# Performance work log

Measured on AMD Instinct MI355X. Metric: run time of the kernel, lower is better.

## Reference

```python
import jax, jax.numpy as jnp
import numpy as np

B, L, C = 131072, 50, 3
WIN = 10  # running std window


def setup_inputs() -> dict:
    key = jax.random.key(0)
    ks = jax.random.split(key, 12)
    def xavier(k, shape, fan_in, fan_out, gain):
        bound = gain * np.sqrt(6.0 / (fan_in + fan_out))
        return jax.random.uniform(k, shape, jnp.float32, -bound, bound)
    relu_g = np.sqrt(2.0)
    return {
        "signal": jax.random.normal(ks[0], (B, L, C), jnp.float32),
        # conv weights: (out_ch, in_ch, kernel)
        "conv1_w": xavier(ks[1], (5, 3, 3), 3 * 3, 5 * 3, relu_g),
        "conv1_b": jnp.zeros((5,), jnp.float32),
        "conv2_w": xavier(ks[2], (10, 5, 3), 5 * 3, 10 * 3, relu_g),
        "conv2_b": jnp.zeros((10,), jnp.float32),
        "fc1_w": xavier(ks[3], (256, 360), 360, 256, relu_g),
        "fc1_b": jnp.zeros((256,), jnp.float32),
        "fc2_w": xavier(ks[4], (64, 256), 256, 64, relu_g),
        "fc2_b": jnp.zeros((64,), jnp.float32),
        "pamap_w": xavier(ks[5], (12, 64), 64, 12, 1.0),
        "pamap_b": jnp.zeros((12,), jnp.float32),
    }


def running_std(x, w):
    # x: (B, L, C) -> (B, L - w, C); unbiased std (ddof=1) over sliding window,
    # computed with prefix sums instead of per-window kernels.
    b, l, c = x.shape
    z = jnp.zeros((b, 1, c), x.dtype)
    cs = jnp.concatenate([z, jnp.cumsum(x, axis=1)], axis=1)
    cs2 = jnp.concatenate([z, jnp.cumsum(x * x, axis=1)], axis=1)
    lo = l - w  # note: torch loop produces L - w windows (last window dropped)
    s = cs[:, w:w + lo] - cs[:, :lo]
    s2 = cs2[:, w:w + lo] - cs2[:, :lo]
    var = (s2 - s * s / w) / (w - 1)
    return jnp.sqrt(jnp.maximum(var, 0.0))


def conv1d(x, w, b):
    # x: (B, C, T), w: (O, I, K)
    y = jax.lax.conv_general_dilated(x, w, (1,), 'VALID',
                                     dimension_numbers=('NCH', 'OIH', 'NCH'))
    return y + b[None, :, None]


def reference(signal, conv1_w, conv1_b, conv2_w, conv2_b,
              fc1_w, fc1_b, fc2_w, fc2_b, pamap_w, pamap_b):
    sd = running_std(signal, WIN)            # (B, 40, 3)
    x = jnp.transpose(sd, (0, 2, 1))          # (B, 3, 40)
    h = jax.nn.relu(conv1d(x, conv1_w, conv1_b))   # (B, 5, 38)
    h = jax.nn.relu(conv1d(h, conv2_w, conv2_b))   # (B, 10, 36)
    flat = jnp.transpose(h, (0, 2, 1)).reshape(-1, 36 * 10)  # (B, 360)
    f = jax.nn.relu(flat @ fc1_w.T + fc1_b)
    f = jax.nn.relu(f @ fc2_w.T + fc2_b)
    logits = f @ pamap_w.T + pamap_b           # flag=False -> pamap head
    return jax.nn.log_softmax(logits, axis=1)
```

## Files before the change

### kernel.cpp

```cpp
#include <hip/hip_runtime.h>
#include <hip/hip_bf16.h>

typedef __attribute__((ext_vector_type(8))) short bf16x8;
typedef __attribute__((ext_vector_type(4))) float f32x4;
typedef __attribute__((ext_vector_type(8))) unsigned short u16x8;

static __device__ __forceinline__ unsigned short bf16bits(float v) {
    __hip_bfloat16 h = __float2bfloat16(v);
    return *(unsigned short*)&h;
}

__global__ __launch_bounds__(256) void prep_weights(
    const float* __restrict__ fc1w, const float* __restrict__ fc2w,
    __hip_bfloat16* __restrict__ w1o, __hip_bfloat16* __restrict__ w2o)
{
    int id = blockIdx.x * 256 + threadIdx.x;
    if (id < 256 * 384) {
        int n = id / 384, k2 = id - n * 384;
        float v = 0.0f;
        if (k2 < 360) {
            int o = k2 / 36, t = k2 - o * 36;
            v = fc1w[n * 360 + t * 10 + o];
        }
        w1o[id] = __float2bfloat16(v);
    } else {
        int id2 = id - 256 * 384;
        if (id2 < 64 * 256) w2o[id2] = __float2bfloat16(fc2w[id2]);
    }
}

#define P_BASE  0
#define P_TILE  10496
#define P_SSTR  656
#define SD_BASE 20992
#define SD_TILE 11008
#define SD_SSTR 688
#define F_BASE  20992
#define F_RSTR  784
#define CW_OFF  46080
__global__ __launch_bounds__(256, 3) void features_kernel(
    const float* __restrict__ sig,
    const float* __restrict__ c1w_g, const float* __restrict__ c1b_g,
    const float* __restrict__ c2w_g, const float* __restrict__ c2b_g,
    __hip_bfloat16* __restrict__ Fg)
{
    __shared__ __align__(16) unsigned char smem[46920];
    float* cw = (float*)(smem + CW_OFF);

    const int tid  = threadIdx.x;
    const int blk  = blockIdx.x;
    const int wv   = tid >> 6;
    const int lane = tid & 63;
    const int ml   = lane & 15;
    const int kg   = lane >> 4;

    {
        f32x4 z = {0.f, 0.f, 0.f, 0.f};
        for (int i = tid; i < 2688; i += 256)
            *(f32x4*)(smem + i * 16) = z;
        if (tid < 210) {
            float v;
            if (tid < 45)       v = c1w_g[tid];
            else if (tid < 50)  v = c1b_g[tid - 45];
            else if (tid < 200) v = c2w_g[tid - 50];
            else                v = c2b_g[tid - 200];
            cw[tid] = v;
        }
    }
    __syncthreads();

    if (tid < 192) {
        int s = tid / 6, r = tid - s * 6;
        int c = r >> 1, h = r & 1;
        int j0 = h * 20;
        const float* g = sig + (size_t)blk * 4800 + s * 150 + c;
        float x[30];
        #pragma unroll
        for (int j = 0; j < 30; ++j) x[j] = g[(j0 + j) * 3];
        float sum = 0.f, sq = 0.f;
        #pragma unroll
        for (int j = 0; j < 10; ++j) { sum += x[j]; sq += x[j] * x[j]; }
        unsigned char* sd = smem + SD_BASE + (s >> 4) * SD_TILE + (s & 15) * SD_SSTR + c * 2;
        #pragma unroll
        for (int i = 0; i < 20; ++i) {
            float var = (sq - sum * sum * 0.1f) * (1.0f / 9.0f);
            *(unsigned short*)(sd + (j0 + i) * 16) = bf16bits(sqrtf(fmaxf(var, 0.f)));
            if (i < 19) {
                float d = x[i + 10] - x[i];
                sq  += d * (x[i + 10] + x[i]);
                sum += d;
            }
        }
    }

    bf16x8 B1f, B2f;
    #pragma unroll
    for (int j = 0; j < 8; ++j) {
        float v1 = (ml < 5  && kg < 3 && j < 3) ? cw[ml * 9 + j * 3 + kg] : 0.f;
        float v2 = (ml < 10 && kg < 3 && j < 5) ? cw[50 + ml * 15 + j * 3 + kg] : 0.f;
        B1f[j] = (short)bf16bits(v1);
        B2f[j] = (short)bf16bits(v2);
    }
    const float c1bias = (ml < 5)  ? cw[45 + ml]  : 0.f;
    const float c2bias = (ml < 10) ? cw[200 + ml] : 0.f;
    __syncthreads();

    {
        const int tile = wv >> 1, half = wv & 1;
        const unsigned char* sdb = smem + SD_BASE + tile * SD_TILE + ml * SD_SSTR;
        unsigned char* pb = smem + P_BASE + tile * P_TILE + ml * 2;
        #pragma unroll
        for (int it = 0; it < 19; ++it) {
            int t = half * 19 + it;
            bf16x8 a = *(const bf16x8*)(sdb + (t + kg) * 16);
            f32x4 acc = {0.f, 0.f, 0.f, 0.f};
            acc = __builtin_amdgcn_mfma_f32_16x16x32_bf16(a, B1f, acc, 0, 0, 0);
            if (ml < 5) {
                #pragma unroll
                for (int i = 0; i < 4; ++i) {
                    float v = fmaxf(acc[i] + c1bias, 0.f);
                    *(unsigned short*)(pb + (kg * 4 + i) * P_SSTR + t * 16) = bf16bits(v);
                }
            }
        }
    }
    __syncthreads();

    if (tid < 128) {
        f32x4 z = {0.f, 0.f, 0.f, 0.f};
        int r = tid >> 2, q = tid & 3;
        *(f32x4*)(smem + F_BASE + r * F_RSTR + 720 + q * 16) = z;
    }

    {
        const int tile = wv >> 1, half = wv & 1;
        const unsigned char* pbr = smem + P_BASE + tile * P_TILE + ml * P_SSTR;
        unsigned char* fb = smem + F_BASE + tile * 16 * F_RSTR + ml * 72;
        #pragma unroll
        for (int it = 0; it < 18; ++it) {
            int t = half * 18 + it;
            bf16x8 a = *(const bf16x8*)(pbr + (t + kg) * 16);
            f32x4 acc = {0.f, 0.f, 0.f, 0.f};
            acc = __builtin_amdgcn_mfma_f32_16x16x32_bf16(a, B2f, acc, 0, 0, 0);
            if (ml < 10) {
                #pragma unroll
                for (int i = 0; i < 4; ++i) {
                    float v = fmaxf(acc[i] + c2bias, 0.f);
                    *(unsigned short*)(fb + (kg * 4 + i) * F_RSTR + t * 2) = bf16bits(v);
                }
            }
        }
    }
    __syncthreads();

    {
        u16x8* dstv = (u16x8*)Fg + (size_t)blk * 1536;
        for (int i = tid; i < 1536; i += 256) {
            int r = i / 48, cc = i - r * 48;
            dstv[i] = *(const u16x8*)(smem + F_BASE + r * F_RSTR + cc * 16);
        }
    }
}

__global__ __launch_bounds__(256, 2) void fc_head_kernel(
    const __hip_bfloat16* __restrict__ Fg,
    const __hip_bfloat16* __restrict__ W1, const __hip_bfloat16* __restrict__ W2,
    const float* __restrict__ fc1b, const float* __restrict__ fc2b,
    const float* __restrict__ pw, const float* __restrict__ pb,
    float* __restrict__ out)
{
    __shared__ __align__(16) unsigned char smem[63536];
    float* pwl = (float*)(smem + 60416);
    float* pbl = (float*)(smem + 63488);

    const int tid  = threadIdx.x;
    const int blk  = blockIdx.x;
    const int w    = tid >> 6;
    const int lane = tid & 63;
    const int ml   = lane & 15;
    const int kg   = lane >> 4;
    unsigned char* Tw = smem + 50176 + w * 2560;

    for (int i = tid; i < 780; i += 256) {
        if (i < 768) pwl[i] = pw[i]; else pbl[i - 768] = pb[i - 768];
    }

    const __hip_bfloat16* myF = Fg + (size_t)(blk * 128 + w * 32 + ml) * 384;
    bf16x8 bfr[12][2];
    #pragma unroll
    for (int kk = 0; kk < 12; ++kk) {
        bfr[kk][0] = *(const bf16x8*)(myF + kk * 32 + kg * 8);
        bfr[kk][1] = *(const bf16x8*)(myF + 16 * 384 + kk * 32 + kg * 8);
    }

    {
        const u16x8* src = (const u16x8*)W1;
        __hip_bfloat16* b0 = (__hip_bfloat16*)smem;
        #pragma unroll
        for (int it = 0; it < 6; ++it) {
            int v = tid + it * 256;
            int n = v / 48, k8 = v - n * 48;
            *(u16x8*)(b0 + n * 392 + k8 * 8) = src[v];
        }
    }
    bf16x8 a2f[4];
    #pragma unroll
    for (int t2 = 0; t2 < 4; ++t2)
        a2f[t2] = *(const bf16x8*)(W2 + (t2 * 16 + ml) * 256 + kg * 8);

    f32x4 acc2[4][2];
    #pragma unroll
    for (int t2 = 0; t2 < 4; ++t2) {
        acc2[t2][0] = f32x4{0, 0, 0, 0};
        acc2[t2][1] = f32x4{0, 0, 0, 0};
    }

    for (int c = 0; c < 8; ++c) {
        __syncthreads();
        const __hip_bfloat16* cur = (const __hip_bfloat16*)(smem + (c & 1) * 25088);

        u16x8 nf[6];
        bf16x8 a2n[4];
        if (c < 7) {
            const u16x8* src = (const u16x8*)(W1 + (c + 1) * 32 * 384);
            #pragma unroll
            for (int it = 0; it < 6; ++it) nf[it] = src[tid + it * 256];
            #pragma unroll
            for (int t2 = 0; t2 < 4; ++t2)
                a2n[t2] = *(const bf16x8*)(W2 + (t2 * 16 + ml) * 256 + (c + 1) * 32 + kg * 8);
        }

        f32x4 a1acc[2][2];
        #pragma unroll
        for (int rt = 0; rt < 2; ++rt) {
            a1acc[rt][0] = f32x4{0, 0, 0, 0};
            a1acc[rt][1] = f32x4{0, 0, 0, 0};
        }
        #pragma unroll
        for (int kk = 0; kk < 12; ++kk) {
            bf16x8 w0 = *(const bf16x8*)(cur + ml * 392 + kk * 32 + kg * 8);
            bf16x8 w1 = *(const bf16x8*)(cur + (16 + ml) * 392 + kk * 32 + kg * 8);
            a1acc[0][0] = __builtin_amdgcn_mfma_f32_16x16x32_bf16(w0, bfr[kk][0], a1acc[0][0], 0, 0, 0);
            a1acc[0][1] = __builtin_amdgcn_mfma_f32_16x16x32_bf16(w0, bfr[kk][1], a1acc[0][1], 0, 0, 0);
            a1acc[1][0] = __builtin_amdgcn_mfma_f32_16x16x32_bf16(w1, bfr[kk][0], a1acc[1][0], 0, 0, 0);
            a1acc[1][1] = __builtin_amdgcn_mfma_f32_16x16x32_bf16(w1, bfr[kk][1], a1acc[1][1], 0, 0, 0);
        }

        #pragma unroll
        for (int rt = 0; rt < 2; ++rt) {
            float4 b4 = *(const float4*)(fc1b + c * 32 + rt * 16 + kg * 4);
            #pragma unroll
            for (int st = 0; st < 2; ++st) {
                unsigned int p0 =
                    (unsigned int)bf16bits(fmaxf(a1acc[rt][st][0] + b4.x, 0.f))
                  | ((unsigned int)bf16bits(fmaxf(a1acc[rt][st][1] + b4.y, 0.f)) << 16);
                unsigned int p1 =
                    (unsigned int)bf16bits(fmaxf(a1acc[rt][st][2] + b4.z, 0.f))
                  | ((unsigned int)bf16bits(fmaxf(a1acc[rt][st][3] + b4.w, 0.f)) << 16);
                uint2 pk = {p0, p1};
                *(uint2*)(Tw + (st * 16 + ml) * 80 + (rt * 16 + kg * 4) * 2) = pk;
            }
        }
        asm volatile("s_waitcnt lgkmcnt(0)" ::: "memory");
        __builtin_amdgcn_sched_barrier(0);

        bf16x8 pf0 = *(const bf16x8*)(Tw + ml * 80 + kg * 16);
        bf16x8 pf1 = *(const bf16x8*)(Tw + (16 + ml) * 80 + kg * 16);
        #pragma unroll
        for (int t2 = 0; t2 < 4; ++t2) {
            acc2[t2][0] = __builtin_amdgcn_mfma_f32_16x16x32_bf16(a2f[t2], pf0, acc2[t2][0], 0, 0, 0);
            acc2[t2][1] = __builtin_amdgcn_mfma_f32_16x16x32_bf16(a2f[t2], pf1, acc2[t2][1], 0, 0, 0);
        }

        if (c < 7) {
            __hip_bfloat16* nxt = (__hip_bfloat16*)(smem + ((c + 1) & 1) * 25088);
            #pragma unroll
            for (int it = 0; it < 6; ++it) {
                int v = tid + it * 256;
                int n = v / 48, k8 = v - n * 48;
                *(u16x8*)(nxt + n * 392 + k8 * 8) = nf[it];
            }
            #pragma unroll
            for (int t2 = 0; t2 < 4; ++t2) a2f[t2] = a2n[t2];
        }
    }

    #pragma unroll
    for (int st = 0; st < 2; ++st) {
        float h[16];
        #pragma unroll
        for (int t2 = 0; t2 < 4; ++t2) {
            float4 b4 = *(const float4*)(fc2b + t2 * 16 + kg * 4);
            #pragma unroll
            for (int i = 0; i < 4; ++i)
                h[t2 * 4 + i] = fmaxf(acc2[t2][st][i] + ((const float*)&b4)[i], 0.f);
        }
        float lg[12];
        #pragma unroll
        for (int j = 0; j < 12; ++j) {
            float s = 0.f;
            #pragma unroll
            for (int t2 = 0; t2 < 4; ++t2) {
                float4 wv4 = *(const float4*)(pwl + j * 64 + t2 * 16 + kg * 4);
                s += wv4.x * h[t2 * 4 + 0] + wv4.y * h[t2 * 4 + 1]
                   + wv4.z * h[t2 * 4 + 2] + wv4.w * h[t2 * 4 + 3];
            }
            lg[j] = s;
        }
        #pragma unroll
        for (int j = 0; j < 12; ++j) {
            lg[j] += __shfl_xor(lg[j], 16);
            lg[j] += __shfl_xor(lg[j], 32);
            lg[j] += pbl[j];
        }
        float m = lg[0];
        #pragma unroll
        for (int j = 1; j < 12; ++j) m = fmaxf(m, lg[j]);
        float e = 0.f;
        #pragma unroll
        for (int j = 0; j < 12; ++j) e += __expf(lg[j] - m);
        float lse = m + __logf(e);
        if (kg == 0) {
            float* op = out + (size_t)(blk * 128 + w * 32 + st * 16 + ml) * 12;
            float4 o0 = {lg[0] - lse, lg[1] - lse, lg[2]  - lse, lg[3]  - lse};
            float4 o1 = {lg[4] - lse, lg[5] - lse, lg[6]  - lse, lg[7]  - lse};
            float4 o2 = {lg[8] - lse, lg[9] - lse, lg[10] - lse, lg[11] - lse};
            ((float4*)op)[0] = o0; ((float4*)op)[1] = o1; ((float4*)op)[2] = o2;
        }
    }
}

extern "C" void kernel_launch(void* const* d_in, const int* in_sizes, int n_in,
                              void* d_out, int out_size, void* d_ws, size_t ws_size,
                              hipStream_t stream) {
    const float* sig = (const float*)d_in[0];
    const float* c1w = (const float*)d_in[1];
    const float* c1b = (const float*)d_in[2];
    const float* c2w = (const float*)d_in[3];
    const float* c2b = (const float*)d_in[4];
    const float* f1w = (const float*)d_in[5];
    const float* f1b = (const float*)d_in[6];
    const float* f2w = (const float*)d_in[7];
    const float* f2b = (const float*)d_in[8];
    const float* pw  = (const float*)d_in[9];
    const float* pb  = (const float*)d_in[10];
    float* out = (float*)d_out;

    __hip_bfloat16* W1 = (__hip_bfloat16*)d_ws;
    __hip_bfloat16* W2 = (__hip_bfloat16*)((char*)d_ws + 196608);
    __hip_bfloat16* Fg = (__hip_bfloat16*)((char*)d_ws + 229376);

    prep_weights<<<448, 256, 0, stream>>>(f1w, f2w, W1, W2);
    features_kernel<<<4096, 256, 0, stream>>>(sig, c1w, c1b, c2w, c2b, Fg);
    fc_head_kernel<<<1024, 256, 0, stream>>>(Fg, W1, W2, f1b, f2b, pw, pb, out);
}
```

Before: 219.8 us.

## Fuse conv feature kernel with FC head to drop feature round-trip

Merges the features kernel and the FC head kernel into one launch. The bf16 feature tile now stays in LDS and feeds the fc1 MFMA directly, with fc1 output going through LDS to fc2 and the softmax head. This removes the global write and read of the 131072x384 feature matrix and one kernel launch. In exchange, each block now handles only 32 rows and reads the full fc1 weight straight from global/L2 with no LDS staging, so weight traffic per row rises. Only two of the four waves do the fc2 stage, which may leave the CU underused there.

```diff
diff --git a/kernel.cpp b/kernel.cpp
--- a/kernel.cpp
+++ b/kernel.cpp
@@ -38,14 +38,27 @@
 #define F_BASE  20992
 #define F_RSTR  784
 #define CW_OFF  46080
-__global__ __launch_bounds__(256, 3) void features_kernel(
+#define B1B_OFF 46920
+#define B2B_OFF 47944
+#define PW_OFF  48200
+#define PB_OFF  51272
+#define T_BASE  0
+#define T_SSTR  528
+__global__ __launch_bounds__(256, 3) void fused_kernel(
     const float* __restrict__ sig,
     const float* __restrict__ c1w_g, const float* __restrict__ c1b_g,
     const float* __restrict__ c2w_g, const float* __restrict__ c2b_g,
-    __hip_bfloat16* __restrict__ Fg)
+    const __hip_bfloat16* __restrict__ W1, const __hip_bfloat16* __restrict__ W2,
+    const float* __restrict__ fc1b, const float* __restrict__ fc2b,
+    const float* __restrict__ pw, const float* __restrict__ pb,
+    float* __restrict__ out)
 {
-    __shared__ __align__(16) unsigned char smem[46920];
-    float* cw = (float*)(smem + CW_OFF);
+    __shared__ __align__(16) unsigned char smem[51320];
+    float* cw  = (float*)(smem + CW_OFF);
+    float* bb1 = (float*)(smem + B1B_OFF);
+    float* bb2 = (float*)(smem + B2B_OFF);
+    float* pwl = (float*)(smem + PW_OFF);
+    float* pbl = (float*)(smem + PB_OFF);
 
     const int tid  = threadIdx.x;
     const int blk  = blockIdx.x;
@@ -66,6 +79,10 @@
             else                v = c2b_g[tid - 200];
             cw[tid] = v;
         }
+        bb1[tid] = fc1b[tid];
+        if (tid < 64) bb2[tid] = fc2b[tid];
+        for (int i = tid; i < 768; i += 256) pwl[i] = pw[i];
+        if (tid < 12) pbl[tid] = pb[tid];
     }
     __syncthreads();
 
@@ -108,7 +125,7 @@
     {
         const int tile = wv >> 1, half = wv & 1;
         const unsigned char* sdb = smem + SD_BASE + tile * SD_TILE + ml * SD_SSTR;
-        unsigned char* pb = smem + P_BASE + tile * P_TILE + ml * 2;
+        unsigned char* pbuf = smem + P_BASE + tile * P_TILE + ml * 2;
         #pragma unroll
         for (int it = 0; it < 19; ++it) {
             int t = half * 19 + it;
@@ -119,7 +136,7 @@
                 #pragma unroll
                 for (int i = 0; i < 4; ++i) {
                     float v = fmaxf(acc[i] + c1bias, 0.f);
-                    *(unsigned short*)(pb + (kg * 4 + i) * P_SSTR + t * 16) = bf16bits(v);
+                    *(unsigned short*)(pbuf + (kg * 4 + i) * P_SSTR + t * 16) = bf16bits(v);
                 }
             }
         }
@@ -153,147 +170,67 @@
     }
     __syncthreads();
 
-    {
-        u16x8* dstv = (u16x8*)Fg + (size_t)blk * 1536;
-        for (int i = tid; i < 1536; i += 256) {
-            int r = i / 48, cc = i - r * 48;
-            dstv[i] = *(const u16x8*)(smem + F_BASE + r * F_RSTR + cc * 16);
-        }
-    }
-}
-
-__global__ __launch_bounds__(256, 2) void fc_head_kernel(
-    const __hip_bfloat16* __restrict__ Fg,
-    const __hip_bfloat16* __restrict__ W1, const __hip_bfloat16* __restrict__ W2,
-    const float* __restrict__ fc1b, const float* __restrict__ fc2b,
-    const float* __restrict__ pw, const float* __restrict__ pb,
-    float* __restrict__ out)
-{
-    __shared__ __align__(16) unsigned char smem[63536];
-    float* pwl = (float*)(smem + 60416);
-    float* pbl = (float*)(smem + 63488);
-
-    const int tid  = threadIdx.x;
-    const int blk  = blockIdx.x;
-    const int w    = tid >> 6;
-    const int lane = tid & 63;
-    const int ml   = lane & 15;
-    const int kg   = lane >> 4;
-    unsigned char* Tw = smem + 50176 + w * 2560;
-
-    for (int i = tid; i < 780; i += 256) {
-        if (i < 768) pwl[i] = pw[i]; else pbl[i - 768] = pb[i - 768];
-    }
-
-    const __hip_bfloat16* myF = Fg + (size_t)(blk * 128 + w * 32 + ml) * 384;
     bf16x8 bfr[12][2];
     #pragma unroll
     for (int kk = 0; kk < 12; ++kk) {
-        bfr[kk][0] = *(const bf16x8*)(myF + kk * 32 + kg * 8);
-        bfr[kk][1] = *(const bf16x8*)(myF + 16 * 384 + kk * 32 + kg * 8);
-    }
-
-    {
-        const u16x8* src = (const u16x8*)W1;
-        __hip_bfloat16* b0 = (__hip_bfloat16*)smem;
-        #pragma unroll
-        for (int it = 0; it < 6; ++it) {
-            int v = tid + it * 256;
-            int n = v / 48, k8 = v - n * 48;
-            *(u16x8*)(b0 + n * 392 + k8 * 8) = src[v];
-        }
-    }
-    bf16x8 a2f[4];
-    #pragma unroll
-    for (int t2 = 0; t2 < 4; ++t2)
-        a2f[t2] = *(const bf16x8*)(W2 + (t2 * 16 + ml) * 256 + kg * 8);
-
-    f32x4 acc2[4][2];
-    #pragma unroll
-    for (int t2 = 0; t2 < 4; ++t2) {
-        acc2[t2][0] = f32x4{0, 0, 0, 0};
-        acc2[t2][1] = f32x4{0, 0, 0, 0};
-    }
-
-    for (int c = 0; c < 8; ++c) {
-        __syncthreads();
-        const __hip_bfloat16* cur = (const __hip_bfloat16*)(smem + (c & 1) * 25088);
-
-        u16x8 nf[6];
-        bf16x8 a2n[4];
-        if (c < 7) {
-            const u16x8* src = (const u16x8*)(W1 + (c + 1) * 32 * 384);
-            #pragma unroll
-            for (int it = 0; it < 6; ++it) nf[it] = src[tid + it * 256];
-            #pragma unroll
-            for (int t2 = 0; t2 < 4; ++t2)
-                a2n[t2] = *(const bf16x8*)(W2 + (t2 * 16 + ml) * 256 + (c + 1) * 32 + kg * 8);
-        }
-
-        f32x4 a1acc[2][2];
-        #pragma unroll
-        for (int rt = 0; rt < 2; ++rt) {
-            a1acc[rt][0] = f32x4{0, 0, 0, 0};
-            a1acc[rt][1] = f32x4{0, 0, 0, 0};
-        }
-        #pragma unroll
-        for (int kk = 0; kk < 12; ++kk) {
-            bf16x8 w0 = *(const bf16x8*)(cur + ml * 392 + kk * 32 + kg * 8);
-            bf16x8 w1 = *(const bf16x8*)(cur + (16 + ml) * 392 + kk * 32 + kg * 8);
-            a1acc[0][0] = __builtin_amdgcn_mfma_f32_16x16x32_bf16(w0, bfr[kk][0], a1acc[0][0], 0, 0, 0);
-            a1acc[0][1] = __builtin_amdgcn_mfma_f32_16x16x32_bf16(w0, bfr[kk][1], a1acc[0][1], 0, 0, 0);
-            a1acc[1][0] = __builtin_amdgcn_mfma_f32_16x16x32_bf16(w1, bfr[kk][0], a1acc[1][0], 0, 0, 0);
-            a1acc[1][1] = __builtin_amdgcn_mfma_f32_16x16x32_bf16(w1, bfr[kk][1], a1acc[1][1], 0, 0, 0);
-        }
-
-        #pragma unroll
-        for (int rt = 0; rt < 2; ++rt) {
-            float4 b4 = *(const float4*)(fc1b + c * 32 + rt * 16 + kg * 4);
-            #pragma unroll
-            for (int st = 0; st < 2; ++st) {
-                unsigned int p0 =
-                    (unsigned int)bf16bits(fmaxf(a1acc[rt][st][0] + b4.x, 0.f))
-                  | ((unsigned int)bf16bits(fmaxf(a1acc[rt][st][1] + b4.y, 0.f)) << 16);
-                unsigned int p1 =
-                    (unsigned int)bf16bits(fmaxf(a1acc[rt][st][2] + b4.z, 0.f))
-                  | ((unsigned int)bf16bits(fmaxf(a1acc[rt][st][3] + b4.w, 0.f)) << 16);
+        bfr[kk][0] = *(const bf16x8*)(smem + F_BASE + ml * F_RSTR + kk * 64 + kg * 16);
+        bfr[kk][1] = *(const bf16x8*)(smem + F_BASE + (16 + ml) * F_RSTR + kk * 64 + kg * 16);
+    }
+    {
+        const int rowbase = wv * 64;
+        #pragma unroll
+        for (int rt = 0; rt < 4; ++rt) {
+            int row0 = rowbase + rt * 16;
+            const __hip_bfloat16* wsrc = W1 + (size_t)(row0 + ml) * 384 + kg * 8;
+            f32x4 a0 = {0.f, 0.f, 0.f, 0.f}, a1 = {0.f, 0.f, 0.f, 0.f};
+            #pragma unroll
+            for (int kk = 0; kk < 12; ++kk) {
+                bf16x8 wf = *(const bf16x8*)(wsrc + kk * 32);
+                a0 = __builtin_amdgcn_mfma_f32_16x16x32_bf16(wf, bfr[kk][0], a0, 0, 0, 0);
+                a1 = __builtin_amdgcn_mfma_f32_16x16x32_bf16(wf, bfr[kk][1], a1, 0, 0, 0);
+            }
+            float4 b4 = *(const float4*)(bb1 + row0 + kg * 4);
+            {
+                unsigned int p0 = (unsigned int)bf16bits(fmaxf(a0[0] + b4.x, 0.f))
+                                | ((unsigned int)bf16bits(fmaxf(a0[1] + b4.y, 0.f)) << 16);
+                unsigned int p1 = (unsigned int)bf16bits(fmaxf(a0[2] + b4.z, 0.f))
+                                | ((unsigned int)bf16bits(fmaxf(a0[3] + b4.w, 0.f)) << 16);
                 uint2 pk = {p0, p1};
-                *(uint2*)(Tw + (st * 16 + ml) * 80 + (rt * 16 + kg * 4) * 2) = pk;
-            }
-        }
-        asm volatile("s_waitcnt lgkmcnt(0)" ::: "memory");
-        __builtin_amdgcn_sched_barrier(0);
-
-        bf16x8 pf0 = *(const bf16x8*)(Tw + ml * 80 + kg * 16);
-        bf16x8 pf1 = *(const bf16x8*)(Tw + (16 + ml) * 80 + kg * 16);
+                *(uint2*)(smem + T_BASE + ml * T_SSTR + (row0 + kg * 4) * 2) = pk;
+            }
+            {
+                unsigned int p0 = (unsigned int)bf16bits(fmaxf(a1[0] + b4.x, 0.f))
+                                | ((unsigned int)bf16bits(fmaxf(a1[1] + b4.y, 0.f)) << 16);
+                unsigned int p1 = (unsigned int)bf16bits(fmaxf(a1[2] + b4.z, 0.f))
+                                | ((unsigned int)bf16bits(fmaxf(a1[3] + b4.w, 0.f)) << 16);
+                uint2 pk = {p0, p1};
+                *(uint2*)(smem + T_BASE + (16 + ml) * T_SSTR + (row0 + kg * 4) * 2) = pk;
+            }
+        }
+    }
+    __syncthreads();
+
+    if (wv < 2) {
+        f32x4 acc2[4];
+        #pragma unroll
+        for (int t2 = 0; t2 < 4; ++t2) acc2[t2] = f32x4{0.f, 0.f, 0.f, 0.f};
+        #pragma unroll
+        for (int kk = 0; kk < 8; ++kk) {
+            bf16x8 pf = *(const bf16x8*)(smem + T_BASE + (wv * 16 + ml) * T_SSTR
+                                         + (kk * 32 + kg * 8) * 2);
+            #pragma unroll
+            for (int t2 = 0; t2 < 4; ++t2) {
+                bf16x8 a2 = *(const bf16x8*)(W2 + (t2 * 16 + ml) * 256 + kk * 32 + kg * 8);
+                acc2[t2] = __builtin_amdgcn_mfma_f32_16x16x32_bf16(a2, pf, acc2[t2], 0, 0, 0);
+            }
+        }
+        float h[16];
         #pragma unroll
         for (int t2 = 0; t2 < 4; ++t2) {
-            acc2[t2][0] = __builtin_amdgcn_mfma_f32_16x16x32_bf16(a2f[t2], pf0, acc2[t2][0], 0, 0, 0);
-            acc2[t2][1] = __builtin_amdgcn_mfma_f32_16x16x32_bf16(a2f[t2], pf1, acc2[t2][1], 0, 0, 0);
-        }
-
-        if (c < 7) {
-            __hip_bfloat16* nxt = (__hip_bfloat16*)(smem + ((c + 1) & 1) * 25088);
-            #pragma unroll
-            for (int it = 0; it < 6; ++it) {
-                int v = tid + it * 256;
-                int n = v / 48, k8 = v - n * 48;
-                *(u16x8*)(nxt + n * 392 + k8 * 8) = nf[it];
-            }
-            #pragma unroll
-            for (int t2 = 0; t2 < 4; ++t2) a2f[t2] = a2n[t2];
-        }
-    }
-
-    #pragma unroll
-    for (int st = 0; st < 2; ++st) {
-        float h[16];
-        #pragma unroll
-        for (int t2 = 0; t2 < 4; ++t2) {
-            float4 b4 = *(const float4*)(fc2b + t2 * 16 + kg * 4);
+            float4 b4 = *(const float4*)(bb2 + t2 * 16 + kg * 4);
             #pragma unroll
             for (int i = 0; i < 4; ++i)
-                h[t2 * 4 + i] = fmaxf(acc2[t2][st][i] + ((const float*)&b4)[i], 0.f);
+                h[t2 * 4 + i] = fmaxf(acc2[t2][i] + ((const float*)&b4)[i], 0.f);
         }
         float lg[12];
         #pragma unroll
@@ -321,7 +258,7 @@
         for (int j = 0; j < 12; ++j) e += __expf(lg[j] - m);
         float lse = m + __logf(e);
         if (kg == 0) {
-            float* op = out + (size_t)(blk * 128 + w * 32 + st * 16 + ml) * 12;
+            float* op = out + (size_t)(blk * 32 + wv * 16 + ml) * 12;
             float4 o0 = {lg[0] - lse, lg[1] - lse, lg[2]  - lse, lg[3]  - lse};
             float4 o1 = {lg[4] - lse, lg[5] - lse, lg[6]  - lse, lg[7]  - lse};
             float4 o2 = {lg[8] - lse, lg[9] - lse, lg[10] - lse, lg[11] - lse};
@@ -348,9 +285,8 @@
 
     __hip_bfloat16* W1 = (__hip_bfloat16*)d_ws;
     __hip_bfloat16* W2 = (__hip_bfloat16*)((char*)d_ws + 196608);
-    __hip_bfloat16* Fg = (__hip_bfloat16*)((char*)d_ws + 229376);
 
     prep_weights<<<448, 256, 0, stream>>>(f1w, f2w, W1, W2);
-    features_kernel<<<4096, 256, 0, stream>>>(sig, c1w, c1b, c2w, c2b, Fg);
-    fc_head_kernel<<<1024, 256, 0, stream>>>(Fg, W1, W2, f1b, f2b, pw, pb, out);
-}
+    fused_kernel<<<4096, 256, 0, stream>>>(sig, c1w, c1b, c2w, c2b,
+                                           W1, W2, f1b, f2b, pw, pb, out);
+}
```

Result: slower. 297.1 us (+35.2%).
